# Kernel optimization log

Hardware: AMD Instinct MI355X
Metric: run time of the kernel (lower is better)

The kernel has to match this reference:

```python
import jax, jax.numpy as jnp
import numpy as np

IN_DIMS = (32, 64, 96, 128)
N_EXPERTS = len(IN_DIMS)
MAX_F = max(IN_DIMS)
D = 2 * MAX_F
N = 8192
TOP_K = 2
H_DIM = 1024
OUT_DIM = 768
LN_EPS = 1e-6


def _build_mask():
    # mask[f] = [1]*s + [0]*(MAX_F-s) + [1]*s + [0]*(MAX_F-s), shape (E, 1, D)
    m = np.zeros((N_EXPERTS, 1, D), dtype=np.float32)
    for i, s in enumerate(IN_DIMS):
        m[i, 0, :s] = 1.0
        m[i, 0, MAX_F:MAX_F + s] = 1.0
    return jnp.asarray(m)

_MASK = _build_mask()


def _multi_in_expert(x_final, expert_weights, expert_indices, W, b):
    """MoE dispatch/combine of MultiInSizeLinear (expert_indices path).
    x_final: (E, N, D); expert_weights/indices: (N, K); W: (E, O, D); b: (E, O)."""
    Wm = W * _MASK                                   # (E, O, D) masked per-size weights
    # per-expert outputs for every token (the torch loop computes these per mask group)
    Y = jnp.einsum('end,eod->eno', x_final, Wm) + b[:, None, :]   # (E, N, O)
    valid = expert_indices < N_EXPERTS               # (N, K) real-expert mask
    rsum = jnp.sum(expert_weights * valid, axis=-1, keepdims=True)
    rsum = jnp.where(rsum == 0, 1.0, rsum)
    wnorm = jnp.where(valid, expert_weights / rsum, 0.0)          # (N, K)
    safe = jnp.where(valid, expert_indices, 0)
    n_idx = jnp.arange(Y.shape[1])
    gathered = Y[safe, n_idx[:, None]]               # (N, K, O)
    return jnp.sum(wnorm[..., None] * gathered, axis=1)           # (N, O)


def setup_inputs() -> dict:
    key = jax.random.key(0)
    ks = jax.random.split(key, 12)
    s_hid = 1.0 / np.sqrt(D)
    s_out = 1.0 / np.sqrt(H_DIM)
    return {
        'x': jax.random.normal(ks[0], (N, D), jnp.float32),
        'in_feat_size': jax.random.randint(ks[1], (N,), 0, MAX_F, jnp.int64) if jax.config.jax_enable_x64 else jax.random.randint(ks[1], (N,), 0, MAX_F, jnp.int32),
        'expert_weights': jax.random.uniform(ks[2], (N, TOP_K), jnp.float32),
        'expert_indices': jax.random.randint(ks[3], (N, TOP_K), 0, 6, jnp.int32),
        'x_final': jax.random.normal(ks[4], (N_EXPERTS, N, D), jnp.float32),
        'W_hid': jax.random.normal(ks[5], (N_EXPERTS, H_DIM, D), jnp.float32) * s_hid,
        'b_hid': jax.random.normal(ks[6], (N_EXPERTS, H_DIM), jnp.float32) * s_hid,
        'W_out': jax.random.normal(ks[7], (OUT_DIM, H_DIM), jnp.float32) * s_out,
        'b_out': jax.random.normal(ks[8], (OUT_DIM,), jnp.float32) * s_out,
        'W_res': jax.random.normal(ks[9], (N_EXPERTS, OUT_DIM, D), jnp.float32) * s_hid,
        'b_res': jax.random.normal(ks[10], (N_EXPERTS, OUT_DIM), jnp.float32) * s_hid,
        'ln_w': jnp.ones((OUT_DIM,), jnp.float32),
    }


def reference(x, in_feat_size, expert_weights, expert_indices, x_final,
              W_hid, b_hid, W_out, b_out, W_res, b_res, ln_w):
    xf = jnp.nan_to_num(x_final, nan=0.0)
    hid = _multi_in_expert(xf, expert_weights, expert_indices, W_hid, b_hid)
    hid = jax.nn.gelu(hid, approximate=False)
    out = hid @ W_out.T + b_out                      # output_layer (dropout p=0 -> identity)
    res = _multi_in_expert(xf, expert_weights, expert_indices, W_res, b_res)
    out = out + res
    # T5LayerNorm (RMSNorm)
    var = jnp.mean(out * out, axis=-1, keepdims=True)
    return ln_w * (out * jax.lax.rsqrt(var + LN_EPS))
```

## Files before the change

kernel.cpp:

```cpp
#include <hip/hip_runtime.h>
#include <hip/hip_bf16.h>

#define TOKENS 8192
#define D_IN   256
#define HDIM   1024
#define ODIM   768
#define KPACK  704
#define NCHUNK 88

typedef short bf16x8 __attribute__((ext_vector_type(8)));
typedef float f32x4  __attribute__((ext_vector_type(4)));

static __device__ __forceinline__ ushort f2b(float f) {
    union { __hip_bfloat16 b; ushort u; } cv;
    cv.b = __float2bfloat16(f);
    return cv.u;
}
static __device__ __forceinline__ float b2f(ushort u) {
    union { ushort u; __hip_bfloat16 b; } cv;
    cv.u = u;
    return __bfloat162float(cv.b);
}

static __device__ __forceinline__ void chunk_map(int c8, int& e, int& d0) {
    int cc;
    if (c8 < 8)       { e = 0; cc = c8; }
    else if (c8 < 24) { e = 1; cc = c8 - 8; }
    else if (c8 < 48) { e = 2; cc = c8 - 24; }
    else              { e = 3; cc = c8 - 48; }
    int half = 4 * (e + 1);
    d0 = (cc < half) ? cc * 8 : 128 + (cc - half) * 8;
}

static __device__ __forceinline__ void stage16(const ushort* g, ushort* l) {
    __builtin_amdgcn_global_load_lds(
        (const __attribute__((address_space(1))) void*)g,
        (__attribute__((address_space(3))) void*)l, 16, 0, 0);
}

static __device__ __forceinline__ float gelu_f(float v) {
    float y = 0.7978845608f * v * (1.f + 0.044715f * v * v);
    return v - v / (__expf(2.f * y) + 1.f);
}

#define A_ITEMS  (TOKENS * NCHUNK)
#define B_ITEMS  (1792 * NCHUNK)
#define W_ITEMS  (768 * 128)
__global__ __launch_bounds__(256) void k_pack(
    const float* __restrict__ ew, const int* __restrict__ ei,
    const float* __restrict__ xf,
    const float* __restrict__ Whid, const float* __restrict__ bhid,
    const float* __restrict__ Wres, const float* __restrict__ bres,
    const float* __restrict__ Wout,
    ushort* __restrict__ Ap, ushort* __restrict__ Bp, ushort* __restrict__ Wb) {
    int gid = blockIdx.x * 256 + threadIdx.x;
    if (gid < A_ITEMS) {
        int n  = gid / NCHUNK;
        int c8 = gid - n * NCHUNK;
        int   i0 = ei[2 * n], i1 = ei[2 * n + 1];
        float w0 = ew[2 * n], w1 = ew[2 * n + 1];
        bool v0 = (unsigned)i0 < 4u, v1 = (unsigned)i1 < 4u;
        float rs = (v0 ? w0 : 0.f) + (v1 ? w1 : 0.f);
        if (rs == 0.f) rs = 1.f;
        float o0 = v0 ? w0 / rs : 0.f;
        float o1 = v1 ? w1 / rs : 0.f;
        ushort o[8] __attribute__((aligned(16))) = {0, 0, 0, 0, 0, 0, 0, 0};
        if (c8 < 80) {
            int e, d0;
            chunk_map(c8, e, d0);
            float w = ((v0 && i0 == e) ? o0 : 0.f) + ((v1 && i1 == e) ? o1 : 0.f);
            if (w != 0.f) {
                const float* s = xf + ((size_t)e * TOKENS + n) * D_IN + d0;
#pragma unroll
                for (int j = 0; j < 8; ++j) {
                    float v = s[j];
                    if (!(v == v)) v = 0.f;
                    o[j] = f2b(w * v);
                }
            }
        } else if (c8 == 80) {
#pragma unroll
            for (int j = 0; j < 4; ++j) {
                float m = ((v0 && i0 == j) ? o0 : 0.f) + ((v1 && i1 == j) ? o1 : 0.f);
                o[j] = f2b(m);
            }
        }
        *(uint4*)(Ap + (size_t)n * KPACK + c8 * 8) = *(const uint4*)o;
    } else if (gid < A_ITEMS + B_ITEMS) {
        int g2 = gid - A_ITEMS;
        int o_ = g2 / NCHUNK;
        int c8 = g2 - o_ * NCHUNK;
        ushort v[8] __attribute__((aligned(16))) = {0, 0, 0, 0, 0, 0, 0, 0};
        if (c8 < 80) {
            int e, d0;
            chunk_map(c8, e, d0);
            const float* s = (o_ < HDIM)
                ? Whid + ((size_t)e * HDIM + o_) * D_IN + d0
                : Wres + ((size_t)e * ODIM + (o_ - HDIM)) * D_IN + d0;
#pragma unroll
            for (int j = 0; j < 8; ++j) v[j] = f2b(s[j]);
        } else if (c8 == 80) {
#pragma unroll
            for (int j = 0; j < 4; ++j) {
                float b = (o_ < HDIM) ? bhid[j * HDIM + o_] : bres[j * ODIM + (o_ - HDIM)];
                v[j] = f2b(b);
            }
        }
        *(uint4*)(Bp + (size_t)o_ * KPACK + c8 * 8) = *(const uint4*)v;
    } else {
        int g3 = gid - A_ITEMS - B_ITEMS;
        const float* s = Wout + (size_t)g3 * 8;
        ushort v[8] __attribute__((aligned(16)));
#pragma unroll
        for (int j = 0; j < 8; ++j) v[j] = f2b(s[j]);
        *(uint4*)(Wb + (size_t)g3 * 8) = *(const uint4*)v;
    }
}

__global__ __launch_bounds__(256, 2) void k_gemm1(
    const ushort* __restrict__ A, const ushort* __restrict__ B,
    ushort* __restrict__ hidB, ushort* __restrict__ resb) {
    __shared__ __align__(16) ushort As[2][128 * 64];
    __shared__ __align__(16) ushort Bs[2][128 * 64];
    const int tid = threadIdx.x;
    const int lane = tid & 63, w = tid >> 6;
    const int wr = w >> 1, wc = w & 1;
    const int r = lane & 15, g = lane >> 4;
    const int sx = r & 7;

    int bid  = blockIdx.x;
    int widx = (bid & 7) * 112 + (bid >> 3);
    int bm = widx / 14, bn = widx - bm * 14;

    const int srow = tid >> 3;
    const int gc   = (tid & 7) ^ (srow & 7);
    const ushort* Ag = A + (size_t)(bm * 128 + srow) * KPACK + gc * 8;
    const ushort* Bg = B + (size_t)(bn * 128 + srow) * KPACK + gc * 8;
    const int ldst = (w * 8) * 64;

#define G1_STAGE(p, kt) do {                                            \
    _Pragma("unroll")                                                   \
    for (int i_ = 0; i_ < 4; ++i_) {                                    \
        stage16(Ag + (size_t)(i_ * 32) * KPACK + (kt), &As[p][ldst + i_ * 32 * 64]); \
        stage16(Bg + (size_t)(i_ * 32) * KPACK + (kt), &Bs[p][ldst + i_ * 32 * 64]); \
    } } while (0)

    G1_STAGE(0, 0);
    G1_STAGE(1, 64);

    f32x4 acc[4][4] = {};
    const int cA = (wr * 64 + r) * 64;
    const int cB = (wc * 64 + r) * 64;
    const int cs0 = ((0 * 4 + g) ^ sx) * 8;
    const int cs1 = ((1 * 4 + g) ^ sx) * 8;

    int cur = 0;
#pragma unroll
    for (int t = 0; t < 11; ++t) {
        if (t < 10) asm volatile("s_waitcnt vmcnt(8)" ::: "memory");
        else        asm volatile("s_waitcnt vmcnt(0)" ::: "memory");
        __builtin_amdgcn_s_barrier();
        const ushort* Ab = As[cur];
        const ushort* Bb = Bs[cur];
        bf16x8 a0[4], b0[4], a1[4], b1[4];
#pragma unroll
        for (int j = 0; j < 4; ++j) {
            b0[j] = *(const bf16x8*)&Bb[cB + j * 16 * 64 + cs0];
            b1[j] = *(const bf16x8*)&Bb[cB + j * 16 * 64 + cs1];
        }
#pragma unroll
        for (int i = 0; i < 4; ++i) {
            a0[i] = *(const bf16x8*)&Ab[cA + i * 16 * 64 + cs0];
            a1[i] = *(const bf16x8*)&Ab[cA + i * 16 * 64 + cs1];
        }
        asm volatile("s_waitcnt lgkmcnt(0)" ::: "memory");
        __builtin_amdgcn_sched_barrier(0);
        __builtin_amdgcn_s_barrier();
        if (t + 2 < 11) G1_STAGE(cur, (t + 2) * 64);
        __builtin_amdgcn_s_setprio(1);
#pragma unroll
        for (int i = 0; i < 4; ++i)
#pragma unroll
            for (int j = 0; j < 4; ++j)
                acc[i][j] = __builtin_amdgcn_mfma_f32_16x16x32_bf16(
                    a0[i], b0[j], acc[i][j], 0, 0, 0);
#pragma unroll
        for (int i = 0; i < 4; ++i)
#pragma unroll
            for (int j = 0; j < 4; ++j)
                acc[i][j] = __builtin_amdgcn_mfma_f32_16x16x32_bf16(
                    a1[i], b1[j], acc[i][j], 0, 0, 0);
        __builtin_amdgcn_s_setprio(0);
        cur ^= 1;
    }
#undef G1_STAGE

    if (bn < 8) {
#pragma unroll
        for (int fi = 0; fi < 4; ++fi) {
#pragma unroll
            for (int j = 0; j < 4; ++j) {
                int col = bn * 128 + wc * 64 + j * 16 + r;
#pragma unroll
                for (int qq = 0; qq < 4; ++qq) {
                    int row = bm * 128 + wr * 64 + fi * 16 + g * 4 + qq;
                    hidB[(size_t)row * HDIM + col] = f2b(gelu_f(acc[fi][j][qq]));
                }
            }
        }
    } else {
#pragma unroll
        for (int fi = 0; fi < 4; ++fi) {
#pragma unroll
            for (int j = 0; j < 4; ++j) {
                int col = (bn - 8) * 128 + wc * 64 + j * 16 + r;
#pragma unroll
                for (int qq = 0; qq < 4; ++qq) {
                    int row = bm * 128 + wr * 64 + fi * 16 + g * 4 + qq;
                    resb[(size_t)row * ODIM + col] = f2b(acc[fi][j][qq]);
                }
            }
        }
    }
}

__global__ __launch_bounds__(256, 2) void k_gemm2(
    const ushort* __restrict__ A, const ushort* __restrict__ B,
    const float* __restrict__ bout, const ushort* __restrict__ resb,
    ushort* __restrict__ outb) {
    __shared__ __align__(16) ushort As[2][128 * 64];
    __shared__ __align__(16) ushort Bs[2][128 * 64];
    const int tid = threadIdx.x;
    const int lane = tid & 63, w = tid >> 6;
    const int wr = w >> 1, wc = w & 1;
    const int r = lane & 15, g = lane >> 4;

    int bid  = blockIdx.x;
    int widx = (bid & 7) * 48 + (bid >> 3);
    int bm = widx / 6, bn = widx - bm * 6;

    const int srow = tid >> 3;
    const int gc   = (tid & 7) ^ (srow & 7);
    const ushort* Ag = A + (size_t)(bm * 128 + srow) * HDIM + gc * 8;
    const ushort* Bg = B + (size_t)(bn * 128 + srow) * HDIM + gc * 8;
    const int ldst = (w * 8) * 64;

#define G2_STAGE(p, kt) do {                                            \
    _Pragma("unroll")                                                   \
    for (int i_ = 0; i_ < 4; ++i_) {                                    \
        stage16(Ag + (size_t)(i_ * 32) * HDIM + (kt), &As[p][ldst + i_ * 32 * 64]); \
        stage16(Bg + (size_t)(i_ * 32) * HDIM + (kt), &Bs[p][ldst + i_ * 32 * 64]); \
    } } while (0)

    G2_STAGE(0, 0);
    G2_STAGE(1, 64);

    f32x4 acc[4][4] = {};
    const int cA = (wr * 64 + r) * 64;
    const int cB = (wc * 64 + r) * 64;
    const int sx = r & 7;
    const int cs0 = ((0 * 4 + g) ^ sx) * 8;
    const int cs1 = ((1 * 4 + g) ^ sx) * 8;

    int cur = 0;
#pragma unroll
    for (int t = 0; t < 16; ++t) {
        if (t < 15) asm volatile("s_waitcnt vmcnt(8)" ::: "memory");
        else        asm volatile("s_waitcnt vmcnt(0)" ::: "memory");
        __builtin_amdgcn_s_barrier();
        const ushort* Ab = As[cur];
        const ushort* Bb = Bs[cur];
        bf16x8 a0[4], b0[4], a1[4], b1[4];
#pragma unroll
        for (int j = 0; j < 4; ++j) {
            b0[j] = *(const bf16x8*)&Bb[cB + j * 16 * 64 + cs0];
            b1[j] = *(const bf16x8*)&Bb[cB + j * 16 * 64 + cs1];
        }
#pragma unroll
        for (int i = 0; i < 4; ++i) {
            a0[i] = *(const bf16x8*)&Ab[cA + i * 16 * 64 + cs0];
            a1[i] = *(const bf16x8*)&Ab[cA + i * 16 * 64 + cs1];
        }
        asm volatile("s_waitcnt lgkmcnt(0)" ::: "memory");
        __builtin_amdgcn_sched_barrier(0);
        __builtin_amdgcn_s_barrier();
        if (t + 2 < 16) G2_STAGE(cur, (t + 2) * 64);
        __builtin_amdgcn_s_setprio(1);
#pragma unroll
        for (int i = 0; i < 4; ++i)
#pragma unroll
            for (int j = 0; j < 4; ++j)
                acc[i][j] = __builtin_amdgcn_mfma_f32_16x16x32_bf16(
                    a0[i], b0[j], acc[i][j], 0, 0, 0);
#pragma unroll
        for (int i = 0; i < 4; ++i)
#pragma unroll
            for (int j = 0; j < 4; ++j)
                acc[i][j] = __builtin_amdgcn_mfma_f32_16x16x32_bf16(
                    a1[i], b1[j], acc[i][j], 0, 0, 0);
        __builtin_amdgcn_s_setprio(0);
        cur ^= 1;
    }
#undef G2_STAGE

#pragma unroll
    for (int fi = 0; fi < 4; ++fi) {
#pragma unroll
        for (int j = 0; j < 4; ++j) {
            int col = bn * 128 + wc * 64 + j * 16 + r;
#pragma unroll
            for (int qq = 0; qq < 4; ++qq) {
                int row = bm * 128 + wr * 64 + fi * 16 + g * 4 + qq;
                size_t idx = (size_t)row * ODIM + col;
                float v = acc[fi][j][qq] + bout[col] + b2f(resb[idx]);
                outb[idx] = f2b(v);
            }
        }
    }
}

__global__ __launch_bounds__(256) void k_rms(
    const ushort* __restrict__ outb, const float* __restrict__ lnw,
    float* __restrict__ out) {
    int row = blockIdx.x, t = threadIdx.x;
    const ushort* p = outb + (size_t)row * ODIM;
    float v0 = b2f(p[t]), v1 = b2f(p[t + 256]), v2 = b2f(p[t + 512]);
    float s = v0 * v0 + v1 * v1 + v2 * v2;
#pragma unroll
    for (int off = 32; off > 0; off >>= 1) s += __shfl_down(s, off, 64);
    __shared__ float ws4[4];
    if ((t & 63) == 0) ws4[t >> 6] = s;
    __syncthreads();
    float tot = ws4[0] + ws4[1] + ws4[2] + ws4[3];
    float sc = rsqrtf(tot * (1.f / 768.f) + 1e-6f);
    out[(size_t)row * ODIM + t]       = lnw[t]       * v0 * sc;
    out[(size_t)row * ODIM + t + 256] = lnw[t + 256] * v1 * sc;
    out[(size_t)row * ODIM + t + 512] = lnw[t + 512] * v2 * sc;
}

extern "C" void kernel_launch(void* const* d_in, const int* in_sizes, int n_in,
                              void* d_out, int out_size, void* d_ws, size_t ws_size,
                              hipStream_t stream) {
    const float* ew   = (const float*)d_in[2];
    const int*   ei   = (const int*)d_in[3];
    const float* xf   = (const float*)d_in[4];
    const float* Whid = (const float*)d_in[5];
    const float* bhid = (const float*)d_in[6];
    const float* Wout = (const float*)d_in[7];
    const float* bout = (const float*)d_in[8];
    const float* Wres = (const float*)d_in[9];
    const float* bres = (const float*)d_in[10];
    const float* lnw  = (const float*)d_in[11];

    char* ws = (char*)d_ws;
    ushort* Ap   = (ushort*)(ws);
    ushort* Bp   = (ushort*)(ws + 11534336);
    ushort* Wb   = (ushort*)(ws + 14057472);
    ushort* hidB = (ushort*)(ws + 15630336);
    ushort* resb = (ushort*)(ws + 32407552);
    ushort* outb = (ushort*)(ws + 44990464);

    k_pack<<<3816, 256, 0, stream>>>(ew, ei, xf, Whid, bhid, Wres, bres, Wout,
                                     Ap, Bp, Wb);
    k_gemm1<<<896, 256, 0, stream>>>(Ap, Bp, hidB, resb);
    k_gemm2<<<384, 256, 0, stream>>>(hidB, Wb, bout, resb, outb);
    k_rms<<<8192, 256, 0, stream>>>(outb, lnw, (float*)d_out);
}
```

Measured before the change: 67.31 us.

## Make gemm1 persistent over two tiles per block and vectorize RMSNorm rows

k_gemm1 now launches 512 blocks, so every block computes one tile and many compute a second, covering the 896 tiles in a single wave with 2 blocks per CU. The goal is to remove the tail of a partial second wave. A barrier is added between the tiles so shared-memory reuse stays safe. k_rms now handles 8 rows per block, with 32 lanes per row, 16-byte vector loads and stores, and a shuffle-only reduction, which drops the shared-memory reduction and __syncthreads and cuts block count. The risk is that the two-tile blocks serialize, leaving the total load imbalanced.

```diff
diff --git a/kernel.cpp b/kernel.cpp
--- a/kernel.cpp
+++ b/kernel.cpp
@@ -127,16 +127,25 @@
     const int wr = w >> 1, wc = w & 1;
     const int r = lane & 15, g = lane >> 4;
     const int sx = r & 7;
-
-    int bid  = blockIdx.x;
-    int widx = (bid & 7) * 112 + (bid >> 3);
-    int bm = widx / 14, bn = widx - bm * 14;
-
+    const int cs0 = ((0 * 4 + g) ^ sx) * 8;
+    const int cs1 = ((1 * 4 + g) ^ sx) * 8;
     const int srow = tid >> 3;
     const int gc   = (tid & 7) ^ (srow & 7);
-    const ushort* Ag = A + (size_t)(bm * 128 + srow) * KPACK + gc * 8;
-    const ushort* Bg = B + (size_t)(bn * 128 + srow) * KPACK + gc * 8;
     const int ldst = (w * 8) * 64;
+    const int cA = (wr * 64 + r) * 64;
+    const int cB = (wc * 64 + r) * 64;
+
+    const int xcd = blockIdx.x & 7, j = blockIdx.x >> 3;
+
+    for (int ti = 0; ti < 2; ++ti) {
+        int local = (ti == 0) ? j : (j < 48 ? 64 + j : -1);
+        if (local < 0) break;
+        int widx = xcd * 112 + local;
+        int bm = widx / 14, bn = widx - bm * 14;
+        if (ti == 1) __builtin_amdgcn_s_barrier();
+
+        const ushort* Ag = A + (size_t)(bm * 128 + srow) * KPACK + gc * 8;
+        const ushort* Bg = B + (size_t)(bn * 128 + srow) * KPACK + gc * 8;
 
 #define G1_STAGE(p, kt) do {                                            \
     _Pragma("unroll")                                                   \
@@ -145,79 +154,75 @@
         stage16(Bg + (size_t)(i_ * 32) * KPACK + (kt), &Bs[p][ldst + i_ * 32 * 64]); \
     } } while (0)
 
-    G1_STAGE(0, 0);
-    G1_STAGE(1, 64);
-
-    f32x4 acc[4][4] = {};
-    const int cA = (wr * 64 + r) * 64;
-    const int cB = (wc * 64 + r) * 64;
-    const int cs0 = ((0 * 4 + g) ^ sx) * 8;
-    const int cs1 = ((1 * 4 + g) ^ sx) * 8;
-
-    int cur = 0;
-#pragma unroll
-    for (int t = 0; t < 11; ++t) {
-        if (t < 10) asm volatile("s_waitcnt vmcnt(8)" ::: "memory");
-        else        asm volatile("s_waitcnt vmcnt(0)" ::: "memory");
-        __builtin_amdgcn_s_barrier();
-        const ushort* Ab = As[cur];
-        const ushort* Bb = Bs[cur];
-        bf16x8 a0[4], b0[4], a1[4], b1[4];
-#pragma unroll
-        for (int j = 0; j < 4; ++j) {
-            b0[j] = *(const bf16x8*)&Bb[cB + j * 16 * 64 + cs0];
-            b1[j] = *(const bf16x8*)&Bb[cB + j * 16 * 64 + cs1];
-        }
-#pragma unroll
-        for (int i = 0; i < 4; ++i) {
-            a0[i] = *(const bf16x8*)&Ab[cA + i * 16 * 64 + cs0];
-            a1[i] = *(const bf16x8*)&Ab[cA + i * 16 * 64 + cs1];
-        }
-        asm volatile("s_waitcnt lgkmcnt(0)" ::: "memory");
-        __builtin_amdgcn_sched_barrier(0);
-        __builtin_amdgcn_s_barrier();
-        if (t + 2 < 11) G1_STAGE(cur, (t + 2) * 64);
-        __builtin_amdgcn_s_setprio(1);
-#pragma unroll
-        for (int i = 0; i < 4; ++i)
-#pragma unroll
-            for (int j = 0; j < 4; ++j)
-                acc[i][j] = __builtin_amdgcn_mfma_f32_16x16x32_bf16(
-                    a0[i], b0[j], acc[i][j], 0, 0, 0);
-#pragma unroll
-        for (int i = 0; i < 4; ++i)
-#pragma unroll
-            for (int j = 0; j < 4; ++j)
-                acc[i][j] = __builtin_amdgcn_mfma_f32_16x16x32_bf16(
-                    a1[i], b1[j], acc[i][j], 0, 0, 0);
-        __builtin_amdgcn_s_setprio(0);
-        cur ^= 1;
-    }
+        G1_STAGE(0, 0);
+        G1_STAGE(1, 64);
+
+        f32x4 acc[4][4] = {};
+        int cur = 0;
+#pragma unroll
+        for (int t = 0; t < 11; ++t) {
+            if (t < 10) asm volatile("s_waitcnt vmcnt(8)" ::: "memory");
+            else        asm volatile("s_waitcnt vmcnt(0)" ::: "memory");
+            __builtin_amdgcn_s_barrier();
+            const ushort* Ab = As[cur];
+            const ushort* Bb = Bs[cur];
+            bf16x8 a0[4], b0[4], a1[4], b1[4];
+#pragma unroll
+            for (int jj = 0; jj < 4; ++jj) {
+                b0[jj] = *(const bf16x8*)&Bb[cB + jj * 16 * 64 + cs0];
+                b1[jj] = *(const bf16x8*)&Bb[cB + jj * 16 * 64 + cs1];
+            }
+#pragma unroll
+            for (int i = 0; i < 4; ++i) {
+                a0[i] = *(const bf16x8*)&Ab[cA + i * 16 * 64 + cs0];
+                a1[i] = *(const bf16x8*)&Ab[cA + i * 16 * 64 + cs1];
+            }
+            asm volatile("s_waitcnt lgkmcnt(0)" ::: "memory");
+            __builtin_amdgcn_sched_barrier(0);
+            __builtin_amdgcn_s_barrier();
+            if (t + 2 < 11) G1_STAGE(cur, (t + 2) * 64);
+            __builtin_amdgcn_s_setprio(1);
+#pragma unroll
+            for (int i = 0; i < 4; ++i)
+#pragma unroll
+                for (int jj = 0; jj < 4; ++jj)
+                    acc[i][jj] = __builtin_amdgcn_mfma_f32_16x16x32_bf16(
+                        a0[i], b0[jj], acc[i][jj], 0, 0, 0);
+#pragma unroll
+            for (int i = 0; i < 4; ++i)
+#pragma unroll
+                for (int jj = 0; jj < 4; ++jj)
+                    acc[i][jj] = __builtin_amdgcn_mfma_f32_16x16x32_bf16(
+                        a1[i], b1[jj], acc[i][jj], 0, 0, 0);
+            __builtin_amdgcn_s_setprio(0);
+            cur ^= 1;
+        }
 #undef G1_STAGE
 
-    if (bn < 8) {
-#pragma unroll
-        for (int fi = 0; fi < 4; ++fi) {
-#pragma unroll
-            for (int j = 0; j < 4; ++j) {
-                int col = bn * 128 + wc * 64 + j * 16 + r;
-#pragma unroll
-                for (int qq = 0; qq < 4; ++qq) {
-                    int row = bm * 128 + wr * 64 + fi * 16 + g * 4 + qq;
-                    hidB[(size_t)row * HDIM + col] = f2b(gelu_f(acc[fi][j][qq]));
+        if (bn < 8) {
+#pragma unroll
+            for (int fi = 0; fi < 4; ++fi) {
+#pragma unroll
+                for (int jj = 0; jj < 4; ++jj) {
+                    int col = bn * 128 + wc * 64 + jj * 16 + r;
+#pragma unroll
+                    for (int qq = 0; qq < 4; ++qq) {
+                        int row = bm * 128 + wr * 64 + fi * 16 + g * 4 + qq;
+                        hidB[(size_t)row * HDIM + col] = f2b(gelu_f(acc[fi][jj][qq]));
+                    }
                 }
             }
-        }
-    } else {
-#pragma unroll
-        for (int fi = 0; fi < 4; ++fi) {
-#pragma unroll
-            for (int j = 0; j < 4; ++j) {
-                int col = (bn - 8) * 128 + wc * 64 + j * 16 + r;
-#pragma unroll
-                for (int qq = 0; qq < 4; ++qq) {
-                    int row = bm * 128 + wr * 64 + fi * 16 + g * 4 + qq;
-                    resb[(size_t)row * ODIM + col] = f2b(acc[fi][j][qq]);
+        } else {
+#pragma unroll
+            for (int fi = 0; fi < 4; ++fi) {
+#pragma unroll
+                for (int jj = 0; jj < 4; ++jj) {
+                    int col = (bn - 8) * 128 + wc * 64 + jj * 16 + r;
+#pragma unroll
+                    for (int qq = 0; qq < 4; ++qq) {
+                        int row = bm * 128 + wr * 64 + fi * 16 + g * 4 + qq;
+                        resb[(size_t)row * ODIM + col] = f2b(acc[fi][jj][qq]);
+                    }
                 }
             }
         }
@@ -272,9 +277,9 @@
         const ushort* Bb = Bs[cur];
         bf16x8 a0[4], b0[4], a1[4], b1[4];
 #pragma unroll
-        for (int j = 0; j < 4; ++j) {
-            b0[j] = *(const bf16x8*)&Bb[cB + j * 16 * 64 + cs0];
-            b1[j] = *(const bf16x8*)&Bb[cB + j * 16 * 64 + cs1];
+        for (int jj = 0; jj < 4; ++jj) {
+            b0[jj] = *(const bf16x8*)&Bb[cB + jj * 16 * 64 + cs0];
+            b1[jj] = *(const bf16x8*)&Bb[cB + jj * 16 * 64 + cs1];
         }
 #pragma unroll
         for (int i = 0; i < 4; ++i) {
@@ -289,15 +294,15 @@
 #pragma unroll
         for (int i = 0; i < 4; ++i)
 #pragma unroll
-            for (int j = 0; j < 4; ++j)
-                acc[i][j] = __builtin_amdgcn_mfma_f32_16x16x32_bf16(
-                    a0[i], b0[j], acc[i][j], 0, 0, 0);
+            for (int jj = 0; jj < 4; ++jj)
+                acc[i][jj] = __builtin_amdgcn_mfma_f32_16x16x32_bf16(
+                    a0[i], b0[jj], acc[i][jj], 0, 0, 0);
 #pragma unroll
         for (int i = 0; i < 4; ++i)
 #pragma unroll
-            for (int j = 0; j < 4; ++j)
-                acc[i][j] = __builtin_amdgcn_mfma_f32_16x16x32_bf16(
-                    a1[i], b1[j], acc[i][j], 0, 0, 0);
+            for (int jj = 0; jj < 4; ++jj)
+                acc[i][jj] = __builtin_amdgcn_mfma_f32_16x16x32_bf16(
+                    a1[i], b1[jj], acc[i][jj], 0, 0, 0);
         __builtin_amdgcn_s_setprio(0);
         cur ^= 1;
     }
@@ -306,13 +311,13 @@
 #pragma unroll
     for (int fi = 0; fi < 4; ++fi) {
 #pragma unroll
-        for (int j = 0; j < 4; ++j) {
-            int col = bn * 128 + wc * 64 + j * 16 + r;
+        for (int jj = 0; jj < 4; ++jj) {
+            int col = bn * 128 + wc * 64 + jj * 16 + r;
 #pragma unroll
             for (int qq = 0; qq < 4; ++qq) {
                 int row = bm * 128 + wr * 64 + fi * 16 + g * 4 + qq;
                 size_t idx = (size_t)row * ODIM + col;
-                float v = acc[fi][j][qq] + bout[col] + b2f(resb[idx]);
+                float v = acc[fi][jj][qq] + bout[col] + b2f(resb[idx]);
                 outb[idx] = f2b(v);
             }
         }
@@ -322,20 +327,44 @@
 __global__ __launch_bounds__(256) void k_rms(
     const ushort* __restrict__ outb, const float* __restrict__ lnw,
     float* __restrict__ out) {
-    int row = blockIdx.x, t = threadIdx.x;
+    int t = threadIdx.x;
+    int lr = t >> 5, lc = t & 31;
+    int row = blockIdx.x * 8 + lr;
     const ushort* p = outb + (size_t)row * ODIM;
-    float v0 = b2f(p[t]), v1 = b2f(p[t + 256]), v2 = b2f(p[t + 512]);
-    float s = v0 * v0 + v1 * v1 + v2 * v2;
-#pragma unroll
-    for (int off = 32; off > 0; off >>= 1) s += __shfl_down(s, off, 64);
-    __shared__ float ws4[4];
-    if ((t & 63) == 0) ws4[t >> 6] = s;
-    __syncthreads();
-    float tot = ws4[0] + ws4[1] + ws4[2] + ws4[3];
-    float sc = rsqrtf(tot * (1.f / 768.f) + 1e-6f);
-    out[(size_t)row * ODIM + t]       = lnw[t]       * v0 * sc;
-    out[(size_t)row * ODIM + t + 256] = lnw[t + 256] * v1 * sc;
-    out[(size_t)row * ODIM + t + 512] = lnw[t + 512] * v2 * sc;
+    float v[24];
+    float s = 0.f;
+#pragma unroll
+    for (int c = 0; c < 3; ++c) {
+        uint4 q = *(const uint4*)(p + (lc + 32 * c) * 8);
+        const ushort* u = (const ushort*)&q;
+#pragma unroll
+        for (int k = 0; k < 8; ++k) {
+            float f = b2f(u[k]);
+            v[c * 8 + k] = f;
+            s += f * f;
+        }
+    }
+#pragma unroll
+    for (int off = 16; off > 0; off >>= 1) s += __shfl_xor(s, off, 32);
+    float sc = rsqrtf(s * (1.f / 768.f) + 1e-6f);
+    float* o = out + (size_t)row * ODIM;
+#pragma unroll
+    for (int c = 0; c < 3; ++c) {
+        int base = (lc + 32 * c) * 8;
+        float4 l0 = *(const float4*)&lnw[base];
+        float4 l1 = *(const float4*)&lnw[base + 4];
+        float4 w0, w1;
+        w0.x = l0.x * v[c * 8 + 0] * sc;
+        w0.y = l0.y * v[c * 8 + 1] * sc;
+        w0.z = l0.z * v[c * 8 + 2] * sc;
+        w0.w = l0.w * v[c * 8 + 3] * sc;
+        w1.x = l1.x * v[c * 8 + 4] * sc;
+        w1.y = l1.y * v[c * 8 + 5] * sc;
+        w1.z = l1.z * v[c * 8 + 6] * sc;
+        w1.w = l1.w * v[c * 8 + 7] * sc;
+        *(float4*)&o[base]     = w0;
+        *(float4*)&o[base + 4] = w1;
+    }
 }
 
 extern "C" void kernel_launch(void* const* d_in, const int* in_sizes, int n_in,
@@ -362,7 +391,7 @@
 
     k_pack<<<3816, 256, 0, stream>>>(ew, ei, xf, Whid, bhid, Wres, bres, Wout,
                                      Ap, Bp, Wb);
-    k_gemm1<<<896, 256, 0, stream>>>(Ap, Bp, hidB, resb);
+    k_gemm1<<<512, 256, 0, stream>>>(Ap, Bp, hidB, resb);
     k_gemm2<<<384, 256, 0, stream>>>(hidB, Wb, bout, resb, outb);
-    k_rms<<<8192, 256, 0, stream>>>(outb, lnw, (float*)d_out);
-}
+    k_rms<<<1024, 256, 0, stream>>>(outb, lnw, (float*)d_out);
+}
```

New measurement: 69.26 us. 1.03x slower.
